# Performance work log

Hardware: AMD Instinct MI355X
Metric: run time of the kernel (lower is better)

Reference implementation:

```python
import jax, jax.numpy as jnp
import numpy as np

EPS = 1e-6
K_MEM, C_MEM = 512, 2048
SEQ, BATCH = 256, 16
NUM_LAYERS, NUM_HEADS, HEAD_DIM = 12, 12, 64
KV_DIM = NUM_LAYERS * NUM_HEADS * HEAD_DIM * 2  # 18432
NOISE_STD = 0.01
PINV_STEPS = 3
BEN_COHEN_INIT = -5.0


def approx_pinv(A, steps=PINV_STEPS):
    # Ben-Cohen iterative pseudoinverse. A: (B, M, N) -> (B, N, M)
    alpha = jnp.minimum(jnp.exp(jnp.float32(BEN_COHEN_INIT)), jnp.float32(5e-4))  # clamp(max=5e-4)
    P = alpha * jnp.swapaxes(A, -2, -1)
    for _ in range(steps):
        P = 2.0 * P - (P @ A) @ P  # matches bmm(bmm(P, A), P)
    return P


def setup_inputs() -> dict:
    key = jax.random.key(0)
    ks = jax.random.split(key, 6)
    lim = np.sqrt(6.0 / (C_MEM + KV_DIM))  # xavier_uniform
    return {
        "z_sequence": jax.random.normal(ks[0], (SEQ, BATCH, C_MEM), jnp.float32),
        "z_query": jax.random.normal(ks[1], (BATCH, C_MEM), jnp.float32),
        "noise": jax.random.normal(ks[2], (SEQ, BATCH, C_MEM), jnp.float32),
        "memory_mean": jax.random.normal(ks[3], (K_MEM, C_MEM), jnp.float32) * 0.02,
        "memory_logvar": jnp.zeros((K_MEM,), jnp.float32),
        "w_logvar": jnp.zeros((1,), jnp.float32),
        "W_M_weight": jax.random.uniform(ks[4], (KV_DIM, C_MEM), jnp.float32, -lim, lim),
    }


def reference(z_sequence, z_query, noise, memory_mean, memory_logvar, w_logvar, W_M_weight):
    B = z_query.shape[0]
    # ---- write ----
    prior_var = jnp.exp(memory_logvar) + EPS                     # (K,)
    prior_mean_b = jnp.broadcast_to(memory_mean, (B, K_MEM, C_MEM))
    z_noise = z_sequence + noise * NOISE_STD                     # (S, B, C)
    z_t = jnp.swapaxes(z_noise, 0, 1)                            # (B, S, C)
    M_pinv = approx_pinv(prior_mean_b)                           # (B, C, K)
    w = z_t @ M_pinv                                             # (B, S, K)
    w_pinv = approx_pinv(w)                                      # (B, K, S)
    new_memory_mean = w_pinv @ z_t                               # (B, K, C)
    # KL divergence (post_var == prior_var here)
    t1 = C_MEM * jnp.sum(prior_var / prior_var)
    t2 = jnp.sum((new_memory_mean - prior_mean_b) ** 2 / prior_var[None, :, None], axis=(-2, -1))
    t3 = -jnp.float32(C_MEM * K_MEM)
    t4 = C_MEM * jnp.sum(jnp.log(prior_var) - jnp.log(prior_var))
    dkl_M = jnp.mean(t1 + t2 + t3 + t4)
    # ---- read (deterministic addressing) ----
    M_pinv2 = approx_pinv(new_memory_mean)                       # (B, C, K)
    w_mean = jnp.einsum('bc,bck->bk', z_query, M_pinv2)          # (B, K)
    z_retrieved = jnp.einsum('bk,bkc->bc', w_mean, new_memory_mean)  # (B, C)
    Z_r_kv = z_retrieved @ W_M_weight.T                          # (B, kv_dim)
    wl = jnp.broadcast_to(w_logvar, w_mean.shape)
    dkl_w = 0.5 * jnp.sum(jnp.exp(wl) + w_mean ** 2 - 1.0 - wl)
    return z_retrieved, Z_r_kv, dkl_M, dkl_w
```

## Files before the change

### kernel.cpp

```cpp
#include <hip/hip_runtime.h>

#define ALPHA 5.0e-4f

typedef short s16x8 __attribute__((ext_vector_type(8)));
typedef unsigned short u16x8 __attribute__((ext_vector_type(8)));
typedef float f32x4 __attribute__((ext_vector_type(4)));

__device__ __forceinline__ unsigned short f2bf(float f) {
    unsigned int u = __builtin_bit_cast(unsigned int, f);
    u += 0x7fffu + ((u >> 16) & 1u);
    return (unsigned short)(u >> 16);
}
__device__ __forceinline__ float bf2f(unsigned short h) {
    return __builtin_bit_cast(float, (unsigned int)h << 16);
}
__device__ __forceinline__ f32x4 mfma16(s16x8 a, s16x8 b, f32x4 c) {
    return __builtin_amdgcn_mfma_f32_16x16x32_bf16(a, b, c, 0, 0, 0);
}

template<int ROWS>
__device__ __forceinline__ void stage_kcontig(const float* __restrict__ src, int ld,
                                              unsigned short* __restrict__ lds, int tid)
{
#pragma unroll
    for (int it = 0; it < ROWS * 8 / 256; ++it) {
        const int g = tid + it * 256;
        const int row = g >> 3, s = g & 7;
        const float* p = src + (long long)row * ld + s * 8;
        const float4 x0 = *(const float4*)p;
        const float4 x1 = *(const float4*)(p + 4);
        u16x8 h;
        h[0] = f2bf(x0.x); h[1] = f2bf(x0.y); h[2] = f2bf(x0.z); h[3] = f2bf(x0.w);
        h[4] = f2bf(x1.x); h[5] = f2bf(x1.y); h[6] = f2bf(x1.z); h[7] = f2bf(x1.w);
        *(u16x8*)(lds + row * 64 + ((s ^ (row & 7)) << 3)) = h;
    }
}

template<int ROWS>
__device__ __forceinline__ void stage_kstrided(const float* __restrict__ src, int ld,
                                               unsigned short* __restrict__ lds, int tid)
{
    constexpr int KPT = ROWS * 64 / 256;
    const int m = tid % ROWS, kb = (tid / ROWS) * KPT;
#pragma unroll
    for (int j8 = 0; j8 < KPT / 8; ++j8) {
        u16x8 h;
#pragma unroll
        for (int j = 0; j < 8; ++j)
            h[j] = f2bf(src[(long long)(kb + j8 * 8 + j) * ld + m]);
        const int s = (kb >> 3) + j8;
        *(u16x8*)(lds + m * 64 + ((s ^ (m & 7)) << 3)) = h;
    }
}

template<int ROWS>
__device__ __forceinline__ void stage_kcontig_b(const unsigned short* __restrict__ src, int ld,
                                                unsigned short* __restrict__ lds, int tid)
{
#pragma unroll
    for (int it = 0; it < ROWS * 8 / 256; ++it) {
        const int g = tid + it * 256;
        const int row = g >> 3, s = g & 7;
        const u16x8 h = *(const u16x8*)(src + (long long)row * ld + s * 8);
        *(u16x8*)(lds + row * 64 + ((s ^ (row & 7)) << 3)) = h;
    }
}

template<int ROWS>
__device__ __forceinline__ void stage_kstrided_b(const unsigned short* __restrict__ src, int ld,
                                                 unsigned short* __restrict__ lds, int tid)
{
    constexpr int KPT = ROWS * 64 / 256;
    const int m = tid % ROWS, kb = (tid / ROWS) * KPT;
#pragma unroll
    for (int j8 = 0; j8 < KPT / 8; ++j8) {
        u16x8 h;
#pragma unroll
        for (int j = 0; j < 8; ++j)
            h[j] = src[(long long)(kb + j8 * 8 + j) * ld + m];
        const int s = (kb >> 3) + j8;
        *(u16x8*)(lds + m * 64 + ((s ^ (m & 7)) << 3)) = h;
    }
}

template<int BM, int BN, bool TA, bool TB, bool ABF, bool BBF, bool OBF,
         bool OT, bool CINT>
__device__ __forceinline__
void gemm_dev(int bx, int by, int bz,
              const void* __restrict__ Av, int lda, long long sA,
              const void* __restrict__ Bv, int ldb, long long sB,
              void* __restrict__ Dv, int ldd, long long sD,
              const float* __restrict__ Cin, long long sC,
              float alpha, float beta, int Kd)
{
    constexpr int TWM = BM / 2, TWN = BN / 2;
    constexpr int FM = TWM / 16, FN = TWN / 16;
    __shared__ unsigned short As[BM * 64];
    __shared__ unsigned short Bs[BN * 64];

    const int tid = threadIdx.x;
    const int lane = tid & 63, w = tid >> 6;
    const int wm = w >> 1, wn = w & 1;
    const int lrow = lane & 15, lk = lane >> 4;
    const int m0 = by * BM, n0 = bx * BN;

    f32x4 acc[FM][FN];
#pragma unroll
    for (int i = 0; i < FM; ++i)
#pragma unroll
        for (int j = 0; j < FN; ++j) acc[i][j] = (f32x4){0.f, 0.f, 0.f, 0.f};

    for (int k0 = 0; k0 < Kd; k0 += 64) {
        if (ABF) {
            const unsigned short* Ab = (const unsigned short*)Av + (long long)bz * sA;
            if (!TA) stage_kcontig_b<BM>(Ab + (long long)m0 * lda + k0, lda, As, tid);
            else     stage_kstrided_b<BM>(Ab + (long long)k0 * lda + m0, lda, As, tid);
        } else {
            const float* Ab = (const float*)Av + (long long)bz * sA;
            if (!TA) stage_kcontig<BM>(Ab + (long long)m0 * lda + k0, lda, As, tid);
            else     stage_kstrided<BM>(Ab + (long long)k0 * lda + m0, lda, As, tid);
        }
        if (BBF) {
            const unsigned short* Bb = (const unsigned short*)Bv + (long long)bz * sB;
            if (TB)  stage_kcontig_b<BN>(Bb + (long long)n0 * ldb + k0, ldb, Bs, tid);
            else     stage_kstrided_b<BN>(Bb + (long long)k0 * ldb + n0, ldb, Bs, tid);
        } else {
            const float* Bb = (const float*)Bv + (long long)bz * sB;
            if (TB)  stage_kcontig<BN>(Bb + (long long)n0 * ldb + k0, ldb, Bs, tid);
            else     stage_kstrided<BN>(Bb + (long long)k0 * ldb + n0, ldb, Bs, tid);
        }
        __syncthreads();
#pragma unroll
        for (int kk = 0; kk < 2; ++kk) {
            s16x8 ah[FM], bh[FN];
#pragma unroll
            for (int i = 0; i < FM; ++i) {
                const int row = wm * TWM + i * 16 + lrow;
                const int s = kk * 4 + lk;
                ah[i] = *(const s16x8*)(As + row * 64 + ((s ^ (row & 7)) << 3));
            }
#pragma unroll
            for (int j = 0; j < FN; ++j) {
                const int col = wn * TWN + j * 16 + lrow;
                const int s = kk * 4 + lk;
                bh[j] = *(const s16x8*)(Bs + col * 64 + ((s ^ (col & 7)) << 3));
            }
#pragma unroll
            for (int i = 0; i < FM; ++i)
#pragma unroll
                for (int j = 0; j < FN; ++j)
                    acc[i][j] = mfma16(ah[i], bh[j], acc[i][j]);
        }
        __syncthreads();
    }

#pragma unroll
    for (int i = 0; i < FM; ++i)
#pragma unroll
        for (int j = 0; j < FN; ++j) {
            const int col = n0 + wn * TWN + j * 16 + lrow;
#pragma unroll
            for (int r = 0; r < 4; ++r) {
                const int row = m0 + wm * TWM + i * 16 + lk * 4 + r;
                float v = alpha * acc[i][j][r];
                if (Cin) {
                    const float cv = CINT ? Cin[(long long)col * sC + row]
                                          : Cin[(long long)row * ldd + col];
                    v = fmaf(beta, cv, v);
                }
                if (OT) {
                    ((unsigned short*)Dv)[(long long)(row >> 8) * sD +
                                          (long long)col * ldd + (row & 255)] = f2bf(v);
                } else if (OBF) {
                    ((unsigned short*)Dv + (long long)bz * sD)[(long long)row * ldd + col] = f2bf(v);
                } else {
                    ((float*)Dv + (long long)bz * sD)[(long long)row * ldd + col] = v;
                }
            }
        }
}

template<int BM, int BN, bool TA, bool TB, bool ABF, bool BBF, bool OBF,
         bool OT = false, bool CINT = false>
__global__ __launch_bounds__(256)
void gemm_mfma(const void* __restrict__ Av, int lda, long long sA,
               const void* __restrict__ Bv, int ldb, long long sB,
               void* __restrict__ Dv, int ldd, long long sD,
               const float* __restrict__ Cin, long long sC,
               float alpha, float beta, int Kd)
{
    gemm_dev<BM, BN, TA, TB, ABF, BBF, OBF, OT, CINT>(
        blockIdx.x, blockIdx.y, blockIdx.z,
        Av, lda, sA, Bv, ldb, sB, Dv, ldd, sD, Cin, sC, alpha, beta, Kd);
}

__global__ __launch_bounds__(256)
void fused_prep_kernel(const float* __restrict__ zs, const float* __restrict__ no,
                       const float* __restrict__ zq, const float* __restrict__ mm,
                       unsigned short* __restrict__ ztb, float* __restrict__ q,
                       float* __restrict__ G1, float* __restrict__ wmean,
                       float* __restrict__ out)
{
    const int blk = blockIdx.x, t = threadIdx.x;
    if (blk < 4096) {
        const int bs = blk;
        const int b = bs >> 8, sI = bs & 255;
        const long long in = ((long long)sI * 16 + b) * 2048 + t * 8;
        const f32x4 z0 = __builtin_nontemporal_load((const f32x4*)(zs + in));
        const f32x4 z1 = __builtin_nontemporal_load((const f32x4*)(zs + in + 4));
        const f32x4 n0 = __builtin_nontemporal_load((const f32x4*)(no + in));
        const f32x4 n1 = __builtin_nontemporal_load((const f32x4*)(no + in + 4));
        float zf[8];
#pragma unroll
        for (int j = 0; j < 4; ++j) {
            zf[j]     = fmaf(0.01f, n0[j], z0[j]);
            zf[j + 4] = fmaf(0.01f, n1[j], z1[j]);
        }
        u16x8 o;
#pragma unroll
        for (int j = 0; j < 8; ++j) o[j] = f2bf(zf[j]);
        *(u16x8*)(ztb + ((long long)bs * 2048 + t * 8)) = o;
        const float4 q0 = *(const float4*)(zq + b * 2048 + t * 8);
        const float4 q1 = *(const float4*)(zq + b * 2048 + t * 8 + 4);
        float qa = zf[0] * q0.x + zf[1] * q0.y + zf[2] * q0.z + zf[3] * q0.w
                 + zf[4] * q1.x + zf[5] * q1.y + zf[6] * q1.z + zf[7] * q1.w;
        __shared__ float red[256];
        red[t] = qa; __syncthreads();
        for (int st = 128; st > 0; st >>= 1) { if (t < st) red[t] += red[t + st]; __syncthreads(); }
        if (t == 0) q[bs] = red[0];
    } else if (blk < 4160) {
        const int g = blk - 4096;
        gemm_dev<64, 64, false, true, false, false, false, false, false>(
            g & 7, g >> 3, 0, mm, 2048, 0, mm, 2048, 0, G1, 512, 0,
            nullptr, 0, 1.f, 0.f, 2048);
    } else {
        for (int i = t; i < 8192; i += 256) wmean[i] = 0.f;
        if (t == 0) out[327680] = 0.f;
    }
}

__global__ __launch_bounds__(256)
void wT_u_kernel(const unsigned short* __restrict__ ztb,
                 const unsigned short* __restrict__ P1b,
                 unsigned short* __restrict__ wTb,
                 const float* __restrict__ q, float* __restrict__ wmean)
{
    constexpr int BM = 128, BN = 64, TWM = 64, TWN = 32, FM = 4, FN = 2;
    __shared__ unsigned short As[BM * 64];
    __shared__ unsigned short Bs[BN * 64];
    const int bx = blockIdx.x, by = blockIdx.y;
    const int tid = threadIdx.x;
    const int lane = tid & 63, w = tid >> 6;
    const int wm = w >> 1, wn = w & 1;
    const int lrow = lane & 15, lk = lane >> 4;
    const int m0 = by * BM, n0 = bx * BN;

    f32x4 acc[FM][FN];
#pragma unroll
    for (int i = 0; i < FM; ++i)
#pragma unroll
        for (int j = 0; j < FN; ++j) acc[i][j] = (f32x4){0.f, 0.f, 0.f, 0.f};

    for (int k0 = 0; k0 < 2048; k0 += 64) {
        stage_kcontig_b<BM>(ztb + (long long)m0 * 2048 + k0, 2048, As, tid);
        stage_kstrided_b<BN>(P1b + (long long)k0 * 512 + n0, 512, Bs, tid);
        __syncthreads();
#pragma unroll
        for (int kk = 0; kk < 2; ++kk) {
            s16x8 ah[FM], bh[FN];
#pragma unroll
            for (int i = 0; i < FM; ++i) {
                const int row = wm * TWM + i * 16 + lrow;
                const int s = kk * 4 + lk;
                ah[i] = *(const s16x8*)(As + row * 64 + ((s ^ (row & 7)) << 3));
            }
#pragma unroll
            for (int j = 0; j < FN; ++j) {
                const int col = wn * TWN + j * 16 + lrow;
                const int s = kk * 4 + lk;
                bh[j] = *(const s16x8*)(Bs + col * 64 + ((s ^ (col & 7)) << 3));
            }
#pragma unroll
            for (int i = 0; i < FM; ++i)
#pragma unroll
                for (int j = 0; j < FN; ++j)
                    acc[i][j] = mfma16(ah[i], bh[j], acc[i][j]);
        }
        __syncthreads();
    }

    float up[FN] = {0.f, 0.f};
#pragma unroll
    for (int i = 0; i < FM; ++i)
#pragma unroll
        for (int r = 0; r < 4; ++r) {
            const int row = m0 + wm * TWM + i * 16 + lk * 4 + r;
            const float qv = q[row];
#pragma unroll
            for (int j = 0; j < FN; ++j) {
                const int col = n0 + wn * TWN + j * 16 + lrow;
                const float v = acc[i][j][r];
                wTb[(long long)(row >> 8) * 131072 + (long long)col * 256 + (row & 255)] = f2bf(v);
                up[j] = fmaf(v, qv, up[j]);
            }
        }
    const int b = m0 >> 8;
#pragma unroll
    for (int j = 0; j < FN; ++j) {
        float v = up[j];
        v += __shfl_xor(v, 16);
        v += __shfl_xor(v, 32);
        if (lk == 0) {
            const int col = n0 + wn * TWN + j * 16 + lrow;
            atomicAdd(&wmean[b * 512 + col], (64.0f * ALPHA * ALPHA) * v);
        }
    }
}

__global__ __launch_bounds__(256)
void tail_kernel(const unsigned short* __restrict__ wTb,
                 const unsigned short* __restrict__ ztb,
                 const float* __restrict__ mm, const float* __restrict__ mlv,
                 const float* __restrict__ wmean, const float* __restrict__ wlv,
                 float* __restrict__ out)
{
    __shared__ __align__(16) unsigned char smem[34304];
    const int blk = blockIdx.x, tid = threadIdx.x;
    if (blk < 1024) {
        constexpr int BM = 128, BN = 128, TWM = 64, TWN = 64, FM = 4, FN = 4;
        unsigned short* As = (unsigned short*)smem;
        unsigned short* Bs = As + BM * 64;
        float* ivars = (float*)(smem + 32768);
        float* red = (float*)(smem + 33280);
        const int bx = blk & 15, by = (blk >> 4) & 3, bz = blk >> 6;
        const int lane = tid & 63, w = tid >> 6;
        const int wm = w >> 1, wn = w & 1;
        const int lrow = lane & 15, lk = lane >> 4;
        const int m0 = by * BM, n0 = bx * BN;

        if (tid < 128) ivars[tid] = 1.0f / (expf(mlv[m0 + tid]) + 1e-6f);

        f32x4 acc[FM][FN];
#pragma unroll
        for (int i = 0; i < FM; ++i)
#pragma unroll
            for (int j = 0; j < FN; ++j) acc[i][j] = (f32x4){0.f, 0.f, 0.f, 0.f};

        for (int k0 = 0; k0 < 256; k0 += 64) {
            stage_kcontig_b<BM>(wTb + (long long)bz * 131072 + (long long)m0 * 256 + k0, 256, As, tid);
            stage_kstrided_b<BN>(ztb + (long long)bz * 524288 + (long long)k0 * 2048 + n0, 2048, Bs, tid);
            __syncthreads();
#pragma unroll
            for (int kk = 0; kk < 2; ++kk) {
                s16x8 ah[FM], bh[FN];
#pragma unroll
                for (int i = 0; i < FM; ++i) {
                    const int row = wm * TWM + i * 16 + lrow;
                    const int s = kk * 4 + lk;
                    ah[i] = *(const s16x8*)(As + row * 64 + ((s ^ (row & 7)) << 3));
                }
#pragma unroll
                for (int j = 0; j < FN; ++j) {
                    const int col = wn * TWN + j * 16 + lrow;
                    const int s = kk * 4 + lk;
                    bh[j] = *(const s16x8*)(Bs + col * 64 + ((s ^ (col & 7)) << 3));
                }
#pragma unroll
                for (int i = 0; i < FM; ++i)
#pragma unroll
                    for (int j = 0; j < FN; ++j)
                        acc[i][j] = mfma16(ah[i], bh[j], acc[i][j]);
            }
            __syncthreads();
        }

        const float A8 = 8.0f * ALPHA;
        float da = 0.f;
#pragma unroll
        for (int i = 0; i < FM; ++i)
#pragma unroll
            for (int j = 0; j < FN; ++j) {
                const int cl = wn * TWN + j * 16 + lrow;
#pragma unroll
                for (int r = 0; r < 4; ++r) {
                    const int rl = wm * TWM + i * 16 + lk * 4 + r;
                    const float v = A8 * acc[i][j][r];
                    const float d = v - mm[(long long)(m0 + rl) * 2048 + (n0 + cl)];
                    da = fmaf(d * d, ivars[rl], da);
                }
            }
        red[tid] = da; __syncthreads();
        for (int st = 128; st > 0; st >>= 1) { if (tid < st) red[tid] += red[tid + st]; __syncthreads(); }
        if (tid == 0) atomicAdd(&out[327680], red[0] * (1.0f / 16.0f));
    } else if (blk < 1280) {
        float* wms = (float*)smem;
        float* ys  = (float*)(smem + 2048);
        float* red2 = (float*)(smem + 3072);
        const int idx = blk - 1024, b = idx & 15, ct = idx >> 4;
        wms[tid] = wmean[b * 512 + tid];
        wms[tid + 256] = wmean[b * 512 + 256 + tid];
        __syncthreads();
        {
            const unsigned short* wp = wTb + (long long)b * 131072 + tid;
            float yv = 0.f;
#pragma unroll 8
            for (int k = 0; k < 512; ++k)
                yv = fmaf(wms[k], bf2f(wp[(long long)k * 256]), yv);
            ys[tid] = yv;
        }
        __syncthreads();
        const int c = ct * 128 + (tid & 127), sh = tid >> 7;
        const unsigned short* zp = ztb + (long long)b * 524288 + c;
        float acc2 = 0.f;
        const int sbase = sh * 128;
#pragma unroll 8
        for (int s = 0; s < 128; ++s)
            acc2 = fmaf(ys[sbase + s], bf2f(zp[(long long)(sbase + s) * 2048]), acc2);
        red2[tid] = acc2; __syncthreads();
        if (sh == 0)
            out[(long long)b * 2048 + c] = (8.0f * ALPHA) * (red2[tid] + red2[tid + 128]);
    } else {
        float* red = (float*)smem;
        float s = 0.f;
        for (int i = tid; i < 16 * 512; i += 256) { const float v = wmean[i]; s += v * v; }
        red[tid] = s; __syncthreads();
        for (int st = 128; st > 0; st >>= 1) { if (tid < st) red[tid] += red[tid + st]; __syncthreads(); }
        if (tid == 0) {
            const float l = wlv[0];
            out[327681] = 0.5f * (red[0] + 8192.0f * (expf(l) - 1.0f - l));
        }
    }
}

__global__ __launch_bounds__(256)
void zrkv_mfma_kernel(const float* __restrict__ W, const float* __restrict__ zr,
                      float* __restrict__ part)
{
    const int tid = threadIdx.x, lane = tid & 63, w = tid >> 6;
    const int bx = blockIdx.x, ky = blockIdx.y;
    const int d0 = bx * 64 + w * 16;
    const int kc0 = ky * 256;
    const int rr = lane & 15, kq = lane >> 4;
    s16x8 areg[8];
    const float* zb = zr + rr * 2048 + kc0 + kq * 8;
#pragma unroll
    for (int s = 0; s < 8; ++s) {
        const f32x4 a0 = *(const f32x4*)(zb + s * 32);
        const f32x4 a1 = *(const f32x4*)(zb + s * 32 + 4);
        u16x8 h;
#pragma unroll
        for (int j = 0; j < 4; ++j) { h[j] = f2bf(a0[j]); h[j + 4] = f2bf(a1[j]); }
        areg[s] = __builtin_bit_cast(s16x8, h);
    }
    f32x4 acc = {0.f, 0.f, 0.f, 0.f};
    const float* wb = W + (long long)(d0 + rr) * 2048 + kc0 + kq * 8;
#pragma unroll
    for (int s = 0; s < 8; ++s) {
        const f32x4 b0 = __builtin_nontemporal_load((const f32x4*)(wb + s * 32));
        const f32x4 b1 = __builtin_nontemporal_load((const f32x4*)(wb + s * 32 + 4));
        u16x8 h;
#pragma unroll
        for (int j = 0; j < 4; ++j) { h[j] = f2bf(b0[j]); h[j + 4] = f2bf(b1[j]); }
        acc = mfma16(areg[s], __builtin_bit_cast(s16x8, h), acc);
    }
    float* pb = part + (((long long)ky * 288 + bx) * 4 + w) * 256 + kq * 64 + rr;
#pragma unroll
    for (int r = 0; r < 4; ++r) pb[r * 16] = acc[r];
}

__global__ __launch_bounds__(256)
void zrkv_combine_kernel(const float* __restrict__ part, float* __restrict__ out)
{
    const int b = blockIdx.y;
    const int d = blockIdx.x * 256 + threadIdx.x;
    const int base = ((d >> 6) * 4 + ((d >> 4) & 3)) * 256 + b * 16 + (d & 15);
    float s = 0.f;
#pragma unroll
    for (int ky = 0; ky < 8; ++ky)
        s += part[(long long)ky * 294912 + base];
    out[(long long)b * 18432 + d] = s;
}

extern "C" void kernel_launch(void* const* d_in, const int* in_sizes, int n_in,
                              void* d_out, int out_size, void* d_ws, size_t ws_size,
                              hipStream_t stream)
{
    (void)in_sizes; (void)n_in; (void)out_size; (void)ws_size;
    const float* z_seq   = (const float*)d_in[0];
    const float* z_query = (const float*)d_in[1];
    const float* noise   = (const float*)d_in[2];
    const float* mm      = (const float*)d_in[3];
    const float* mlv     = (const float*)d_in[4];
    const float* wlv     = (const float*)d_in[5];
    const float* WM      = (const float*)d_in[6];
    float* out = (float*)d_out;

    char* wsb = (char*)d_ws;
    unsigned short* ztb  = (unsigned short*)(wsb);
    unsigned short* wTb  = (unsigned short*)(wsb + (16LL << 20));
    float*          G1   = (float*)(wsb + (24LL << 20));
    unsigned short* P1b  = (unsigned short*)(wsb + (26LL << 20));
    float*          pZ   = (float*)(wsb + (40LL << 20));
    float*          vec  = (float*)(wsb + (52LL << 20));
    float* qvec     = vec;
    float* wmean    = vec + 4096;

    fused_prep_kernel<<<4161, 256, 0, stream>>>(z_seq, noise, z_query, mm,
                                                ztb, qvec, G1, wmean, out);
    gemm_mfma<64,64,true,false,false,false,true,false,true><<<dim3(8,32,1),256,0,stream>>>(
        mm,2048,0, G1,512,0, P1b,512,0, mm,2048,
        -28.0f*ALPHA*ALPHA, 8.0f*ALPHA, 512);
    wT_u_kernel<<<dim3(8,32),256,0,stream>>>(ztb, P1b, wTb, qvec, wmean);
    tail_kernel<<<1281,256,0,stream>>>(wTb, ztb, mm, mlv, wmean, wlv, out);
    zrkv_mfma_kernel<<<dim3(288,8),256,0,stream>>>(WM, out, pZ);
    zrkv_combine_kernel<<<dim3(72,16),256,0,stream>>>(pZ, out + 32768);
}
```

Measured before the change: 198.4 us.

## Split-K the Gram GEMM with atomics and remap block indices for L2 locality

The 512x512 Gram matrix of memory_mean, previously computed by 64 blocks each running K=2048, is now split eight ways along K across 512 blocks that accumulate into a zeroed G1 with float atomics. Zeroing of G1, wmean and the KL accumulator moves to hipMemsetAsync calls ahead of the prep kernel. Block indices in wT_u_kernel and the tail kernel are remapped so that neighbouring blocks share operand tiles (same batch or column tile), aiming for better L2/XCD locality. The change adds three memset launches and atomic traffic, and makes the G1 summation order nondeterministic.

Result: faster. 181.4 us (-8.5%).

```diff
diff --git a/kernel.cpp b/kernel.cpp
--- a/kernel.cpp
+++ b/kernel.cpp
@@ -84,7 +84,7 @@
 }
 
 template<int BM, int BN, bool TA, bool TB, bool ABF, bool BBF, bool OBF,
-         bool OT, bool CINT>
+         bool OT, bool CINT, bool ATOM = false>
 __device__ __forceinline__
 void gemm_dev(int bx, int by, int bz,
               const void* __restrict__ Av, int lda, long long sA,
@@ -168,7 +168,9 @@
                                           : Cin[(long long)row * ldd + col];
                     v = fmaf(beta, cv, v);
                 }
-                if (OT) {
+                if (ATOM) {
+                    atomicAdd((float*)Dv + (long long)row * ldd + col, v);
+                } else if (OT) {
                     ((unsigned short*)Dv)[(long long)(row >> 8) * sD +
                                           (long long)col * ldd + (row & 255)] = f2bf(v);
                 } else if (OBF) {
@@ -198,8 +200,7 @@
 void fused_prep_kernel(const float* __restrict__ zs, const float* __restrict__ no,
                        const float* __restrict__ zq, const float* __restrict__ mm,
                        unsigned short* __restrict__ ztb, float* __restrict__ q,
-                       float* __restrict__ G1, float* __restrict__ wmean,
-                       float* __restrict__ out)
+                       float* __restrict__ G1)
 {
     const int blk = blockIdx.x, t = threadIdx.x;
     if (blk < 4096) {
@@ -228,14 +229,14 @@
         red[t] = qa; __syncthreads();
         for (int st = 128; st > 0; st >>= 1) { if (t < st) red[t] += red[t + st]; __syncthreads(); }
         if (t == 0) q[bs] = red[0];
-    } else if (blk < 4160) {
+    } else {
         const int g = blk - 4096;
-        gemm_dev<64, 64, false, true, false, false, false, false, false>(
-            g & 7, g >> 3, 0, mm, 2048, 0, mm, 2048, 0, G1, 512, 0,
-            nullptr, 0, 1.f, 0.f, 2048);
-    } else {
-        for (int i = t; i < 8192; i += 256) wmean[i] = 0.f;
-        if (t == 0) out[327680] = 0.f;
+        const int ky = g & 7;
+        const int tile = g >> 3;
+        gemm_dev<64, 64, false, true, false, false, false, false, false, true>(
+            tile & 7, tile >> 3, 0,
+            mm + ky * 256, 2048, 0, mm + ky * 256, 2048, 0,
+            G1, 512, 0, nullptr, 0, 1.f, 0.f, 256);
     }
 }
 
@@ -248,7 +249,9 @@
     constexpr int BM = 128, BN = 64, TWM = 64, TWN = 32, FM = 4, FN = 2;
     __shared__ unsigned short As[BM * 64];
     __shared__ unsigned short Bs[BN * 64];
-    const int bx = blockIdx.x, by = blockIdx.y;
+    const int lin = blockIdx.x;
+    const int r = lin & 7, tt = lin >> 3;
+    const int by = r + 8 * (tt & 3), bx = tt >> 2;
     const int tid = threadIdx.x;
     const int lane = tid & 63, w = tid >> 6;
     const int wm = w >> 1, wn = w & 1;
@@ -293,13 +296,13 @@
 #pragma unroll
     for (int i = 0; i < FM; ++i)
 #pragma unroll
-        for (int r = 0; r < 4; ++r) {
-            const int row = m0 + wm * TWM + i * 16 + lk * 4 + r;
+        for (int rr = 0; rr < 4; ++rr) {
+            const int row = m0 + wm * TWM + i * 16 + lk * 4 + rr;
             const float qv = q[row];
 #pragma unroll
             for (int j = 0; j < FN; ++j) {
                 const int col = n0 + wn * TWN + j * 16 + lrow;
-                const float v = acc[i][j][r];
+                const float v = acc[i][j][rr];
                 wTb[(long long)(row >> 8) * 131072 + (long long)col * 256 + (row & 255)] = f2bf(v);
                 up[j] = fmaf(v, qv, up[j]);
             }
@@ -332,7 +335,10 @@
         unsigned short* Bs = As + BM * 64;
         float* ivars = (float*)(smem + 32768);
         float* red = (float*)(smem + 33280);
-        const int bx = blk & 15, by = (blk >> 4) & 3, bz = blk >> 6;
+        const int r8 = blk & 7, t8 = blk >> 3;
+        const int bz = r8 + 8 * (t8 & 1);
+        const int rest = t8 >> 1;
+        const int by = rest & 3, bx = rest >> 2;
         const int lane = tid & 63, w = tid >> 6;
         const int wm = w >> 1, wn = w & 1;
         const int lrow = lane & 15, lk = lane >> 4;
@@ -382,9 +388,9 @@
             for (int j = 0; j < FN; ++j) {
                 const int cl = wn * TWN + j * 16 + lrow;
 #pragma unroll
-                for (int r = 0; r < 4; ++r) {
-                    const int rl = wm * TWM + i * 16 + lk * 4 + r;
-                    const float v = A8 * acc[i][j][r];
+                for (int rr = 0; rr < 4; ++rr) {
+                    const int rl = wm * TWM + i * 16 + lk * 4 + rr;
+                    const float v = A8 * acc[i][j][rr];
                     const float d = v - mm[(long long)(m0 + rl) * 2048 + (n0 + cl)];
                     da = fmaf(d * d, ivars[rl], da);
                 }
@@ -396,7 +402,9 @@
         float* wms = (float*)smem;
         float* ys  = (float*)(smem + 2048);
         float* red2 = (float*)(smem + 3072);
-        const int idx = blk - 1024, b = idx & 15, ct = idx >> 4;
+        const int idx = blk - 1024;
+        const int r8 = idx & 7, t8 = idx >> 3;
+        const int b = r8 + 8 * (t8 & 1), ct = t8 >> 1;
         wms[tid] = wmean[b * 512 + tid];
         wms[tid + 256] = wmean[b * 512 + 256 + tid];
         __syncthreads();
@@ -505,12 +513,15 @@
     float* qvec     = vec;
     float* wmean    = vec + 4096;
 
-    fused_prep_kernel<<<4161, 256, 0, stream>>>(z_seq, noise, z_query, mm,
-                                                ztb, qvec, G1, wmean, out);
+    hipMemsetAsync(G1, 0, 512 * 512 * sizeof(float), stream);
+    hipMemsetAsync(wmean, 0, 8192 * sizeof(float), stream);
+    hipMemsetAsync(out + 327680, 0, sizeof(float), stream);
+    fused_prep_kernel<<<4608, 256, 0, stream>>>(z_seq, noise, z_query, mm,
+                                                ztb, qvec, G1);
     gemm_mfma<64,64,true,false,false,false,true,false,true><<<dim3(8,32,1),256,0,stream>>>(
         mm,2048,0, G1,512,0, P1b,512,0, mm,2048,
         -28.0f*ALPHA*ALPHA, 8.0f*ALPHA, 512);
-    wT_u_kernel<<<dim3(8,32),256,0,stream>>>(ztb, P1b, wTb, qvec, wmean);
+    wT_u_kernel<<<256,256,0,stream>>>(ztb, P1b, wTb, qvec, wmean);
     tail_kernel<<<1281,256,0,stream>>>(wTb, ztb, mm, mlv, wmean, wlv, out);
     zrkv_mfma_kernel<<<dim3(288,8),256,0,stream>>>(WM, out, pZ);
     zrkv_combine_kernel<<<dim3(72,16),256,0,stream>>>(pZ, out + 32768);
```
